# Kernel tuning notes

Hardware: AMD Instinct MI355X
Metric: run time of the kernel (lower is better)

## Reference

```python
import math
import jax, jax.numpy as jnp
import numpy as np

G, NP, L = 256, 24, 3            # graphs, atoms per graph, GPS layers
C, TDIM, NFREQ, NT = 256, 256, 10, 100
EDIM = NFREQ * 2 * 3 + 9         # SinusoidsEmbedding.dim + lattice_input_dim = 69
N = G * NP                       # 6144 nodes
H = 4                            # attention heads


def _silu(x):
    return x * jax.nn.sigmoid(x)


def _bn(x, g, b):
    # BatchNorm1d, training-mode batch statistics (biased var), eps=1e-5
    m = x.mean(0)
    v = ((x - m) ** 2).mean(0)
    return (x - m) * jax.lax.rsqrt(v + 1e-5) * g + b


def _forward(t, frac_coords, lattice, type_emb, node_align_W, node_align_b,
             gine_edge_W, gine_edge_b, gine_W1, gine_b1, gine_W2, gine_b2,
             attn_in_W, attn_in_b, attn_out_W, attn_out_b,
             mlp_W1, mlp_b1, mlp_W2, mlp_b2,
             bn1_g, bn1_b, bn2_g, bn2_b, bn3_g, bn3_b, ln_g, ln_b,
             tro_W1, tro_b1, tro_W2, tro_b2,
             lat_W1, lat_b1, lat_W2, lat_b2, lat_W3,
             fc_W1, fc_b1, fc_W2, fc_b2, fc_W3,
             atom_types, node2graph, edge_src, edge_dst):
    # sinusoidal time embedding [G, TDIM], repeated per node
    half = TDIM // 2
    tf = jnp.exp(jnp.arange(half, dtype=jnp.float32) * (-math.log(10000.0) / (half - 1)))
    te = t[:, None] * tf[None, :]
    te = jnp.concatenate([jnp.sin(te), jnp.cos(te)], -1)
    time_emb = jnp.repeat(te, NP, axis=0)                      # [N, TDIM]
    x = jnp.concatenate([type_emb[atom_types], time_emb], 1) @ node_align_W + node_align_b

    # edge features: sinusoids of periodic frac diff + per-graph lattice
    fd = (frac_coords[edge_dst] - frac_coords[edge_src]) % 1.0  # [E,3]
    sf = 2.0 * math.pi * jnp.arange(NFREQ, dtype=jnp.float32)
    emb = (fd[..., None] * sf).reshape(-1, 3 * NFREQ)
    eattr = jnp.concatenate([jnp.sin(emb), jnp.cos(emb), lattice[node2graph[edge_src]]], 1)

    scale = 1.0 / math.sqrt(C // H)
    for l in range(L):
        # --- GINEConv: gather -> relu(x_j + edge_emb) -> scatter-add -> MLP ---
        eemb = eattr @ gine_edge_W[l] + gine_edge_b[l]          # [E, C]
        msg = jax.nn.relu(x[edge_src] + eemb)
        aggr = jax.ops.segment_sum(msg, edge_dst, num_segments=N)
        z = x + aggr                                            # (1+eps)*x, eps=0
        z = _silu(z @ gine_W1[l] + gine_b1[l]) @ gine_W2[l] + gine_b2[l]
        h1 = _bn(z + x, bn1_g[l], bn1_b[l])
        # --- dense-batched multihead self-attention (all graphs have NP nodes) ---
        xd = x.reshape(G, NP, C)
        qkv = xd @ attn_in_W[l] + attn_in_b[l]
        q, k, v = jnp.split(qkv, 3, axis=-1)
        q = q.reshape(G, NP, H, C // H).transpose(0, 2, 1, 3)
        k = k.reshape(G, NP, H, C // H).transpose(0, 2, 1, 3)
        v = v.reshape(G, NP, H, C // H).transpose(0, 2, 1, 3)
        a = jax.nn.softmax(jnp.einsum('ghqd,ghkd->ghqk', q, k) * scale, axis=-1)
        o = jnp.einsum('ghqk,ghkd->ghqd', a, v).transpose(0, 2, 1, 3).reshape(G, NP, C)
        o = (o @ attn_out_W[l] + attn_out_b[l]).reshape(N, C)
        h2 = _bn(o + x, bn2_g[l], bn2_b[l])
        # --- combine + MLP (GPSConv default: ReLU, dropout=0) ---
        out = h1 + h2
        out = out + jax.nn.relu(out @ mlp_W1[l] + mlp_b1[l]) @ mlp_W2[l] + mlp_b2[l]
        x = _bn(out, bn3_g[l], bn3_b[l])

    # final LayerNorm over feature dim
    m = x.mean(-1, keepdims=True)
    v = ((x - m) ** 2).mean(-1, keepdims=True)
    hn = (x - m) * jax.lax.rsqrt(v + 1e-5) * ln_g + ln_b

    # scatter-mean graph pooling
    cnt = jax.ops.segment_sum(jnp.ones((N, 1), hn.dtype), node2graph, num_segments=G)
    gf = jax.ops.segment_sum(hn, node2graph, num_segments=G) / cnt

    types_pred = _silu(hn @ tro_W1 + tro_b1) @ tro_W2 + tro_b2
    lattice_pred = _silu(_silu(gf @ lat_W1 + lat_b1) @ lat_W2 + lat_b2) @ lat_W3
    frac_pred = _silu(_silu(hn @ fc_W1 + fc_b1) @ fc_W2 + fc_b2) @ fc_W3
    return types_pred, lattice_pred, frac_pred


def setup_inputs() -> dict:
    key = jax.random.key(0)
    ki = iter(jax.random.split(key, 40))

    def nrm(shape, s=0.02):
        return jax.random.normal(next(ki), shape, jnp.float32) * s

    # block-diagonal fully-connected edges, dense_to_sparse row-major order
    g = np.repeat(np.arange(G), NP * NP)
    i = np.tile(np.repeat(np.arange(NP), NP), G)
    j = np.tile(np.tile(np.arange(NP), NP), G)
    inp = {
        "t": jax.random.uniform(next(ki), (G,), jnp.float32),
        "frac_coords": jax.random.uniform(next(ki), (N, 3), jnp.float32),
        "lattice": nrm((G, 9), 1.0),
        "type_emb": nrm((NT, C)),
        "node_align_W": nrm((C + TDIM, C)), "node_align_b": jnp.zeros((C,), jnp.float32),
        "gine_edge_W": nrm((L, EDIM, C)), "gine_edge_b": jnp.zeros((L, C), jnp.float32),
        "gine_W1": nrm((L, C, C)), "gine_b1": jnp.zeros((L, C), jnp.float32),
        "gine_W2": nrm((L, C, C)), "gine_b2": jnp.zeros((L, C), jnp.float32),
        "attn_in_W": nrm((L, C, 3 * C)), "attn_in_b": jnp.zeros((L, 3 * C), jnp.float32),
        "attn_out_W": nrm((L, C, C)), "attn_out_b": jnp.zeros((L, C), jnp.float32),
        "mlp_W1": nrm((L, C, 2 * C)), "mlp_b1": jnp.zeros((L, 2 * C), jnp.float32),
        "mlp_W2": nrm((L, 2 * C, C)), "mlp_b2": jnp.zeros((L, C), jnp.float32),
        "bn1_g": jnp.ones((L, C), jnp.float32), "bn1_b": jnp.zeros((L, C), jnp.float32),
        "bn2_g": jnp.ones((L, C), jnp.float32), "bn2_b": jnp.zeros((L, C), jnp.float32),
        "bn3_g": jnp.ones((L, C), jnp.float32), "bn3_b": jnp.zeros((L, C), jnp.float32),
        "ln_g": jnp.ones((C,), jnp.float32), "ln_b": jnp.zeros((C,), jnp.float32),
        "tro_W1": nrm((C, C // 2)), "tro_b1": jnp.zeros((C // 2,), jnp.float32),
        "tro_W2": nrm((C // 2, NT)), "tro_b2": jnp.zeros((NT,), jnp.float32),
        "lat_W1": nrm((C, C // 2)), "lat_b1": jnp.zeros((C // 2,), jnp.float32),
        "lat_W2": nrm((C // 2, C // 4)), "lat_b2": jnp.zeros((C // 4,), jnp.float32),
        "lat_W3": nrm((C // 4, 9)),
        "fc_W1": nrm((C, C // 2)), "fc_b1": jnp.zeros((C // 2,), jnp.float32),
        "fc_W2": nrm((C // 2, C // 4)), "fc_b2": jnp.zeros((C // 4,), jnp.float32),
        "fc_W3": nrm((C // 4, 3)),
        "atom_types": jax.random.randint(next(ki), (N,), 0, NT, jnp.int32),
        "node2graph": jnp.asarray(np.repeat(np.arange(G), NP), jnp.int32),
        "edge_src": jnp.asarray(g * NP + i, jnp.int32),
        "edge_dst": jnp.asarray(g * NP + j, jnp.int32),
    }
    return inp


def reference(t, frac_coords, lattice, type_emb, node_align_W, node_align_b,
              gine_edge_W, gine_edge_b, gine_W1, gine_b1, gine_W2, gine_b2,
              attn_in_W, attn_in_b, attn_out_W, attn_out_b,
              mlp_W1, mlp_b1, mlp_W2, mlp_b2,
              bn1_g, bn1_b, bn2_g, bn2_b, bn3_g, bn3_b, ln_g, ln_b,
              tro_W1, tro_b1, tro_W2, tro_b2,
              lat_W1, lat_b1, lat_W2, lat_b2, lat_W3,
              fc_W1, fc_b1, fc_W2, fc_b2, fc_W3,
              atom_types, node2graph, edge_src, edge_dst):
    return _forward(t, frac_coords, lattice, type_emb, node_align_W, node_align_b,
                    gine_edge_W, gine_edge_b, gine_W1, gine_b1, gine_W2, gine_b2,
                    attn_in_W, attn_in_b, attn_out_W, attn_out_b,
                    mlp_W1, mlp_b1, mlp_W2, mlp_b2,
                    bn1_g, bn1_b, bn2_g, bn2_b, bn3_g, bn3_b, ln_g, ln_b,
                    tro_W1, tro_b1, tro_W2, tro_b2,
                    lat_W1, lat_b1, lat_W2, lat_b2, lat_W3,
                    fc_W1, fc_b1, fc_W2, fc_b2, fc_W3,
                    atom_types, node2graph, edge_src, edge_dst)
```

## Files before the change

### kernel.cpp

```cpp
#include <hip/hip_runtime.h>
#include <hip/hip_bf16.h>
#include <math.h>

#define GG 256
#define NP 24
#define LL 3
#define CC 256
#define NN (GG*NP)
#define HH 4
#define DH 64

typedef __hip_bfloat16 bf;
typedef __attribute__((ext_vector_type(8))) short bfrag;
typedef __attribute__((ext_vector_type(4))) float ffrag;

__device__ __forceinline__ short pk(float x) {
    union { bf h; short s; } u; u.h = __float2bfloat16(x); return u.s;
}
__device__ __forceinline__ float b2f_s(short x) {
    union { short s; bf h; } u; u.s = x; return __bfloat162float(u.h);
}

typedef __attribute__((address_space(1))) const void gv_t;
typedef __attribute__((address_space(3))) void lv_t;

__global__ void signal_k(float* out, int n, float val) {
    int i = blockIdx.x * 256 + threadIdx.x;
    if (i < n) out[i] = val;
}

struct TArgs {
    const float* src[9];
    long dstOff[9];
    int K[9], N[9], L[9];
    int blk0[10];
};
__global__ void transp_all(TArgs a, bf* __restrict__ wt) {
    int bid = blockIdx.x;
    int s = 0;
    while (s < 8 && bid >= a.blk0[s + 1]) ++s;
    long idx = (long)(bid - a.blk0[s]) * 256 + threadIdx.x;
    int KN = a.K[s] * a.N[s];
    long sz = (long)KN * a.L[s];
    if (idx >= sz) return;
    int l = (int)(idx / KN);
    int rem = (int)(idx % KN);
    int k = rem / a.N[s], n = rem % a.N[s];
    wt[a.dstOff[s] + (long)l * KN + (long)n * a.K[s] + k] =
        __float2bfloat16(a.src[s][idx]);
}

#define ETAB_ELEMS (GG * 24 * 24 * 64)
__global__ void prep_gewtab(const float* __restrict__ geW, short* __restrict__ wh,
                            short* __restrict__ wl, const float* __restrict__ frac,
                            short* __restrict__ eh, short* __restrict__ el) {
    int bid = blockIdx.x;
    if (bid < 192) {
        int idx = bid * 256 + threadIdx.x;
        if (idx >= 49152) return;
        int k = idx & 63;
        int n = (idx >> 6) & 127;
        int half = (idx >> 13) & 1;
        int l = idx >> 14;
        float v = (k < 60) ? geW[(long)l * 69 * 256 + (long)k * 256 + half * 128 + n] : 0.f;
        short hi = pk(v);
        short lo = pk(v - b2f_s(hi));
        wh[idx] = hi;
        wl[idx] = lo;
    } else {
        int idx = (bid - 192) * 256 + threadIdx.x;
        if (idx >= ETAB_ELEMS) return;
        int k = idx & 63;
        int rem = idx >> 6;
        int i = rem % 24;
        int rem2 = rem / 24;
        int j = rem2 % 24;
        int g = rem2 / 24;
        float val = 0.f;
        if (k < 60) {
            int r = (k < 30) ? k : k - 30;
            int d = r / 10, f = r % 10;
            float fd = frac[g * 72 + j * 3 + d] - frac[g * 72 + i * 3 + d];
            fd -= floorf(fd);
            float ang = 6.283185307179586f * (float)f * fd;
            val = (k < 30) ? sinf(ang) : cosf(ang);
        }
        short hi = pk(val);
        eh[idx] = hi;
        el[idx] = pk(val - b2f_s(hi));
    }
}

__global__ void build_A(const float* __restrict__ t, const float* __restrict__ type_emb,
                        const unsigned int* __restrict__ atoms,
                        float* __restrict__ A) {
    __shared__ int ok;
    if (threadIdx.x == 0) ok = 1;
    __syncthreads();
    if (atoms[2 * threadIdx.x + 1] != 0u) ok = 0;
    __syncthreads();
    int i64 = ok;
    int idx = blockIdx.x * 256 + threadIdx.x;
    if (idx >= NN * 512) return;
    int n = idx >> 9;
    int k = idx & 511;
    if (k < 256) {
        int a = i64 ? (int)atoms[2 * n] : (int)atoms[n];
        A[idx] = type_emb[(long)a * CC + k];
    } else {
        int d = k - 256;
        int g = n / NP;
        float tv = t[g];
        int dd = (d < 128) ? d : d - 128;
        float tf = expf(dd * (-9.210340371976184f / 127.0f));
        float ang = tv * tf;
        A[idx] = (d < 128) ? sinf(ang) : cosf(ang);
    }
}

__global__ __launch_bounds__(256) void gemm_mfma(
        const float* __restrict__ A, const bf* __restrict__ Wt,
        const float* __restrict__ bias, const float* __restrict__ bias2,
        const float* __restrict__ res,
        float* __restrict__ C, int M, int K, int N, int act) {
    __shared__ __align__(16) short As[2][32 * 72];
    __shared__ __align__(16) short Bs[2][2][64 * 32];
    int tid = threadIdx.x;
    int lane = tid & 63, w = tid >> 6;
    int wm = w & 1, wn = w >> 1;
    int m0 = blockIdx.x * 32, n0 = blockIdx.y * 64;
    ffrag acc[2] = {};
    int sa_m = tid >> 3, sa_k = (tid & 7) << 3;
    int fr_row = lane & 15, quad = lane >> 4, fr_k = quad << 3;
    int brow = w * 16 + (lane >> 2);
    int bko = (lane & 3) << 3;
    const short* wsrc = (const short*)Wt + (long)(n0 + brow) * K + bko;

    {
        const float* Ap = A + (long)(m0 + sa_m) * K + sa_k;
        float4 a1 = *(const float4*)Ap;
        float4 a2 = *(const float4*)(Ap + 4);
        __builtin_amdgcn_global_load_lds((gv_t*)(wsrc), (lv_t*)(&Bs[0][0][w * 512]), 16, 0, 0);
        __builtin_amdgcn_global_load_lds((gv_t*)(wsrc + 32), (lv_t*)(&Bs[0][1][w * 512]), 16, 0, 0);
        short* ap = &As[0][sa_m * 72 + sa_k];
        ap[0] = pk(a1.x); ap[1] = pk(a1.y); ap[2] = pk(a1.z); ap[3] = pk(a1.w);
        ap[4] = pk(a2.x); ap[5] = pk(a2.y); ap[6] = pk(a2.z); ap[7] = pk(a2.w);
    }
    __syncthreads();

    int nk = K >> 6;
    int cur = 0;
    for (int i = 0; i < nk; ++i) {
        float4 a1n, a2n;
        bool more = (i + 1) < nk;
        if (more) {
            int kn = (i + 1) << 6;
            __builtin_amdgcn_global_load_lds((gv_t*)(wsrc + kn),
                (lv_t*)(&Bs[cur ^ 1][0][w * 512]), 16, 0, 0);
            __builtin_amdgcn_global_load_lds((gv_t*)(wsrc + kn + 32),
                (lv_t*)(&Bs[cur ^ 1][1][w * 512]), 16, 0, 0);
            const float* Ap = A + (long)(m0 + sa_m) * K + kn + sa_k;
            a1n = *(const float4*)Ap;
            a2n = *(const float4*)(Ap + 4);
        }
        bfrag af0  = *(const bfrag*)(&As[cur][(wm * 16 + fr_row) * 72 + fr_k]);
        bfrag af1  = *(const bfrag*)(&As[cur][(wm * 16 + fr_row) * 72 + 32 + fr_k]);
        bfrag bg00 = *(const bfrag*)(&Bs[cur][0][(wn * 32 + fr_row) * 32 + fr_k]);
        bfrag bg01 = *(const bfrag*)(&Bs[cur][0][(wn * 32 + 16 + fr_row) * 32 + fr_k]);
        bfrag bg10 = *(const bfrag*)(&Bs[cur][1][(wn * 32 + fr_row) * 32 + fr_k]);
        bfrag bg11 = *(const bfrag*)(&Bs[cur][1][(wn * 32 + 16 + fr_row) * 32 + fr_k]);
        acc[0] = __builtin_amdgcn_mfma_f32_16x16x32_bf16(af0, bg00, acc[0], 0, 0, 0);
        acc[1] = __builtin_amdgcn_mfma_f32_16x16x32_bf16(af0, bg01, acc[1], 0, 0, 0);
        acc[0] = __builtin_amdgcn_mfma_f32_16x16x32_bf16(af1, bg10, acc[0], 0, 0, 0);
        acc[1] = __builtin_amdgcn_mfma_f32_16x16x32_bf16(af1, bg11, acc[1], 0, 0, 0);
        if (more) {
            short* ap = &As[cur ^ 1][sa_m * 72 + sa_k];
            ap[0] = pk(a1n.x); ap[1] = pk(a1n.y); ap[2] = pk(a1n.z); ap[3] = pk(a1n.w);
            ap[4] = pk(a2n.x); ap[5] = pk(a2n.y); ap[6] = pk(a2n.z); ap[7] = pk(a2n.w);
        }
        __syncthreads();
        cur ^= 1;
    }

    int mbase = (lane >> 4) << 2;
#pragma unroll
    for (int nt = 0; nt < 2; ++nt) {
        int n = n0 + wn * 32 + nt * 16 + (lane & 15);
        float bv = bias ? ((bias2 && n >= 128) ? bias2[n - 128] : bias[n]) : 0.f;
#pragma unroll
        for (int r = 0; r < 4; ++r) {
            int m = m0 + wm * 16 + mbase + r;
            float v = acc[nt][r] + bv;
            if (act == 1) v = fmaxf(v, 0.f);
            else if (act == 2) v = v / (1.f + expf(-v));
            if (res) v += res[(long)m * N + n];
            C[(long)m * N + n] = v;
        }
    }
}

__global__ __launch_bounds__(256) void gemm_k(
        const float* __restrict__ A, int lda, const float* __restrict__ W,
        const float* __restrict__ bias, const float* __restrict__ res,
        float* __restrict__ Cf, int M, int K, int Nc, int act) {
    __shared__ __align__(16) float Asf[32][64];
    __shared__ __align__(16) float Bsf[32][64];
    int tid = threadIdx.x;
    int tx = tid & 15, ty = tid >> 4;
    int m0 = blockIdx.x * 64, n0 = blockIdx.y * 64;
    float acc[4][4] = {{0.f}};
    int am = tid >> 2;
    int ak = (tid & 3) << 3;
    int bk = tid >> 4;
    int bn = (tid & 15) << 2;

    for (int k0 = 0; k0 < K; k0 += 32) {
        const float* Ap = A + (long)(m0 + am) * lda + k0 + ak;
        float4 a1 = *(const float4*)Ap;
        float4 a2 = *(const float4*)(Ap + 4);
        float w1[4], w2[4];
#pragma unroll
        for (int u = 0; u < 4; ++u) {
            int n = n0 + bn + u;
            w1[u] = (n < Nc) ? W[(long)(k0 + bk) * Nc + n] : 0.f;
            w2[u] = (n < Nc) ? W[(long)(k0 + bk + 16) * Nc + n] : 0.f;
        }
        __syncthreads();
        Asf[ak + 0][am] = a1.x; Asf[ak + 1][am] = a1.y;
        Asf[ak + 2][am] = a1.z; Asf[ak + 3][am] = a1.w;
        Asf[ak + 4][am] = a2.x; Asf[ak + 5][am] = a2.y;
        Asf[ak + 6][am] = a2.z; Asf[ak + 7][am] = a2.w;
#pragma unroll
        for (int u = 0; u < 4; ++u) {
            Bsf[bk][bn + u] = w1[u];
            Bsf[bk + 16][bn + u] = w2[u];
        }
        __syncthreads();
#pragma unroll
        for (int k = 0; k < 32; ++k) {
            float4 a = *(const float4*)(&Asf[k][ty << 2]);
            float4 b = *(const float4*)(&Bsf[k][tx << 2]);
            acc[0][0] += a.x * b.x; acc[0][1] += a.x * b.y; acc[0][2] += a.x * b.z; acc[0][3] += a.x * b.w;
            acc[1][0] += a.y * b.x; acc[1][1] += a.y * b.y; acc[1][2] += a.y * b.z; acc[1][3] += a.y * b.w;
            acc[2][0] += a.z * b.x; acc[2][1] += a.z * b.y; acc[2][2] += a.z * b.z; acc[2][3] += a.z * b.w;
            acc[3][0] += a.w * b.x; acc[3][1] += a.w * b.y; acc[3][2] += a.w * b.z; acc[3][3] += a.w * b.w;
        }
    }
#pragma unroll
    for (int i = 0; i < 4; ++i) {
        int m = m0 + (ty << 2) + i;
#pragma unroll
        for (int j = 0; j < 4; ++j) {
            int n = n0 + (tx << 2) + j;
            if (n >= Nc) continue;
            float v = acc[i][j];
            if (bias) v += bias[n];
            if (act == 1) v = fmaxf(v, 0.f);
            else if (act == 2) v = v / (1.f + expf(-v));
            if (res) v += res[(long)m * Nc + n];
            Cf[(long)m * Nc + n] = v;
        }
    }
}

#define MF(a, b, c) c = __builtin_amdgcn_mfma_f32_16x16x32_bf16(a, b, c, 0, 0, 0)

__device__ __forceinline__ void stage_etile(const short* __restrict__ ej_h,
                                            const short* __restrict__ ej_l,
                                            short* lds_base, int w, int lane) {
    {
        int c = w;
        const short* src = (c < 3) ? (ej_h + c * 512) : (ej_l + (c - 3) * 512);
        int doff = (c < 3) ? c * 512 : 2048 + (c - 3) * 512;
        __builtin_amdgcn_global_load_lds((gv_t*)(src + lane * 8),
                                         (lv_t*)(lds_base + doff), 16, 0, 0);
    }
    if (w < 2) {
        int c = w + 4;
        const short* src = ej_l + (c - 3) * 512;
        int doff = 2048 + (c - 3) * 512;
        __builtin_amdgcn_global_load_lds((gv_t*)(src + lane * 8),
                                         (lv_t*)(lds_base + doff), 16, 0, 0);
    }
}

__global__ __launch_bounds__(256, 4) void gine4(
        const float* __restrict__ x,
        const float* __restrict__ lattice, const float* __restrict__ geW,
        const float* __restrict__ geb, const short* __restrict__ gewt_h,
        const short* __restrict__ gewt_l, const short* __restrict__ et_h,
        const short* __restrict__ et_l, float* __restrict__ z, int l) {
    __shared__ __align__(16) float xls[24 * 132];
    __shared__ float basel[128];
    __shared__ __align__(16) short ebuf[8192];

    int tid = threadIdx.x;
    int lane = tid & 63, w = tid >> 6, quad = lane >> 4, l16 = lane & 15;
    int g = blockIdx.x >> 2;
    int half = (blockIdx.x >> 1) & 1;
    int jh = blockIdx.x & 1;

    {
        const float4* xg = (const float4*)x;
        for (int idx = tid; idx < 768; idx += 256) {
            int i = idx >> 5, c4 = idx & 31;
            ((float4*)(xls + i * 132))[c4] =
                xg[((long)(g * NP + i) * CC + half * 128) / 4 + c4];
        }
    }
    if (tid < 128) {
        int cg = half * 128 + tid;
        float bv = geb[(long)l * CC + cg];
#pragma unroll
        for (int q = 0; q < 9; ++q)
            bv += lattice[(long)g * 9 + q] * geW[(long)l * 69 * 256 + (long)(60 + q) * 256 + cg];
        basel[tid] = bv;
    }

    bfrag bh00, bh01, bh10, bh11, bl00, bl01, bl10, bl11;
    {
        long base = (long)(l * 2 + half) * 8192;
        int nrow0 = w * 32 + l16;
        int nrow1 = w * 32 + 16 + l16;
        const short* p0h = gewt_h + base + nrow0 * 64 + quad * 8;
        const short* p1h = gewt_h + base + nrow1 * 64 + quad * 8;
        const short* p0l = gewt_l + base + nrow0 * 64 + quad * 8;
        const short* p1l = gewt_l + base + nrow1 * 64 + quad * 8;
        bh00 = *(const bfrag*)(p0h);      bh01 = *(const bfrag*)(p0h + 32);
        bh10 = *(const bfrag*)(p1h);      bh11 = *(const bfrag*)(p1h + 32);
        bl00 = *(const bfrag*)(p0l);      bl01 = *(const bfrag*)(p0l + 32);
        bl10 = *(const bfrag*)(p1l);      bl11 = *(const bfrag*)(p1l + 32);
    }

    const short* ehg = et_h + (long)g * (24 * 24 * 64);
    const short* elg = et_l + (long)g * (24 * 24 * 64);
    int j0 = jh * 12;

    stage_etile(ehg + (long)j0 * 1536, elg + (long)j0 * 1536, ebuf, w, lane);
    __syncthreads();

    float bse0 = basel[w * 32 + l16];
    float bse1 = basel[w * 32 + 16 + l16];

    int cur = 0;
    for (int jc = 0; jc < 12; ++jc) {
        int j = j0 + jc;
        if (jc < 11) {
            stage_etile(ehg + (long)(j + 1) * 1536, elg + (long)(j + 1) * 1536,
                        ebuf + (cur ^ 1) * 4096, w, lane);
        }

        const short* eb = ebuf + cur * 4096;
        int r0 = l16 * 64 + quad * 8;
        int r1 = (16 + l16) * 64 + quad * 8;
        bfrag ah00 = *(const bfrag*)(eb + r0);
        bfrag ah01 = *(const bfrag*)(eb + r0 + 32);
        bfrag ah10 = *(const bfrag*)(eb + r1);
        bfrag ah11 = *(const bfrag*)(eb + r1 + 32);
        bfrag al00 = *(const bfrag*)(eb + 2048 + r0);
        bfrag al01 = *(const bfrag*)(eb + 2048 + r0 + 32);
        bfrag al10 = *(const bfrag*)(eb + 2048 + r1);
        bfrag al11 = *(const bfrag*)(eb + 2048 + r1 + 32);

        ffrag a00 = {}, a01 = {}, a10 = {}, a11 = {};
        MF(ah00, bh00, a00); MF(ah00, bl00, a00); MF(al00, bh00, a00);
        MF(ah00, bh10, a01); MF(ah00, bl10, a01); MF(al00, bh10, a01);
        MF(ah01, bh01, a00); MF(ah01, bl01, a00); MF(al01, bh01, a00);
        MF(ah01, bh11, a01); MF(ah01, bl11, a01); MF(al01, bh11, a01);
        MF(ah10, bh00, a10); MF(ah10, bl00, a10); MF(al10, bh00, a10);
        MF(ah10, bh10, a11); MF(ah10, bl10, a11); MF(al10, bh10, a11);
        MF(ah11, bh01, a10); MF(ah11, bl01, a10); MF(al11, bh01, a10);
        MF(ah11, bh11, a11); MF(ah11, bl11, a11); MF(al11, bh11, a11);

#pragma unroll
        for (int nt = 0; nt < 2; ++nt) {
            int cl = w * 32 + nt * 16 + l16;
            float bse = nt ? bse1 : bse0;
            ffrag am0 = nt ? a01 : a00;
            ffrag am1 = nt ? a11 : a10;
            float part = 0.f;
            {
                int ibase = quad * 4;
#pragma unroll
                for (int r = 0; r < 4; ++r) {
                    float xv = xls[(ibase + r) * 132 + cl];
                    part += fmaxf(xv + bse + am0[r], 0.f);
                }
            }
            if (quad < 2) {
                int ibase = 16 + quad * 4;
#pragma unroll
                for (int r = 0; r < 4; ++r) {
                    float xv = xls[(ibase + r) * 132 + cl];
                    part += fmaxf(xv + bse + am1[r], 0.f);
                }
            }
            part += __shfl_xor(part, 16);
            part += __shfl_xor(part, 32);
            if (lane < 16)
                z[(long)(g * NP + j) * CC + half * 128 + cl] = xls[j * 132 + cl] + part;
        }
        __syncthreads();
        cur ^= 1;
    }
}

__global__ void bn_stats1(const float* __restrict__ in, float* __restrict__ part) {
    int c = threadIdx.x, b = blockIdx.x;
    float s = 0.f, q = 0.f;
    for (int r = 0; r < 64; ++r) {
        float v = in[(long)(b * 64 + r) * CC + c];
        s += v; q += v * v;
    }
    part[b * 512 + c] = s;
    part[b * 512 + 256 + c] = q;
}
__global__ __launch_bounds__(256) void bn_apply2(
        const float* __restrict__ in, const float* __restrict__ part,
        const float* __restrict__ gma, const float* __restrict__ bta,
        const float* __restrict__ add, float* __restrict__ out) {
    int c = threadIdx.x;
    float s = 0.f, q = 0.f;
    for (int b = 0; b < 96; ++b) { s += part[b * 512 + c]; q += part[b * 512 + 256 + c]; }
    float m = s / (float)NN;
    float var = q / (float)NN - m * m;
    float stats_c = m;
    float stats_rs = rsqrtf(var + 1e-5f);
    float gc = gma[c], bc = bta[c];
    for (int r = blockIdx.x; r < NN; r += 768) {
        long idx = (long)r * CC + c;
        float v = (in[idx] - stats_c) * stats_rs * gc + bc;
        if (add) v += add[idx];
        out[idx] = v;
    }
}

__global__ __launch_bounds__(256, 2) void attn2(const float* __restrict__ qkv,
                                                float* __restrict__ o) {
    __shared__ __align__(16) float Kl[24 * 4 * 68];
    __shared__ __align__(16) float Vl[24 * 4 * 68];
    __shared__ float S[4 * 24 * 25];
    int tid = threadIdx.x, g = blockIdx.x;

    const float4* qkv4 = (const float4*)(qkv + (long)g * NP * 768);
    for (int idx = tid; idx < 24 * 128; idx += 256) {
        int row = idx >> 7;
        int c4 = idx & 127;
        int isV = c4 >> 6;
        int cc = c4 & 63;
        int h = cc >> 4, d4 = cc & 15;
        float4 val = qkv4[row * 192 + 64 + c4];
        float* dst = (isV ? Vl : Kl) + (row * 4 + h) * 68 + d4 * 4;
        *(float4*)dst = val;
    }
    __syncthreads();

    if (tid < 96) {
        int h = tid & 3, i = tid >> 2;
        const float4* qp = (const float4*)(qkv + ((long)(g * NP + i)) * 768 + h * 64);
        float4 q[16];
#pragma unroll
        for (int k = 0; k < 16; ++k) q[k] = qp[k];
        float sc[24];
        float mx = -1e30f;
        for (int j = 0; j < 24; ++j) {
            const float4* kp = (const float4*)(Kl + (j * 4 + h) * 68);
            float da = 0.f, db = 0.f;
#pragma unroll
            for (int k = 0; k < 16; k += 2) {
                float4 kv = kp[k];
                da += q[k].x * kv.x; da += q[k].y * kv.y;
                da += q[k].z * kv.z; da += q[k].w * kv.w;
                float4 kv2 = kp[k + 1];
                db += q[k + 1].x * kv2.x; db += q[k + 1].y * kv2.y;
                db += q[k + 1].z * kv2.z; db += q[k + 1].w * kv2.w;
            }
            float s = (da + db) * 0.125f;
            sc[j] = s;
            mx = fmaxf(mx, s);
        }
        float sum = 0.f;
#pragma unroll
        for (int j = 0; j < 24; ++j) { float p = expf(sc[j] - mx); sc[j] = p; sum += p; }
        float inv = 1.f / sum;
#pragma unroll
        for (int j = 0; j < 24; ++j) S[(h * 24 + i) * 25 + j] = sc[j] * inv;
    }
    __syncthreads();

    int h = tid >> 6, d = tid & 63;
    for (int i = 0; i < 24; ++i) {
        const float* Sp = S + (h * 24 + i) * 25;
        float a0 = 0.f, a1 = 0.f;
#pragma unroll
        for (int j = 0; j < 24; j += 2) {
            a0 += Sp[j] * Vl[(j * 4 + h) * 68 + d];
            a1 += Sp[j + 1] * Vl[((j + 1) * 4 + h) * 68 + d];
        }
        o[(long)(g * NP + i) * CC + h * 64 + d] = a0 + a1;
    }
}

__global__ __launch_bounds__(256) void ln_kernel(const float* __restrict__ x,
        const float* __restrict__ gma, const float* __restrict__ bta,
        float* __restrict__ out) {
    __shared__ float red[256];
    int n = blockIdx.x, c = threadIdx.x;
    float v = x[(long)n * CC + c];
    red[c] = v;
    __syncthreads();
    for (int s = 128; s > 0; s >>= 1) { if (c < s) red[c] += red[c + s]; __syncthreads(); }
    float m = red[0] * (1.f / 256.f);
    __syncthreads();
    float dv = v - m;
    red[c] = dv * dv;
    __syncthreads();
    for (int s = 128; s > 0; s >>= 1) { if (c < s) red[c] += red[c + s]; __syncthreads(); }
    float var = red[0] * (1.f / 256.f);
    out[(long)n * CC + c] = dv * rsqrtf(var + 1e-5f) * gma[c] + bta[c];
}

__global__ __launch_bounds__(256) void lat_head(
        const float* __restrict__ hn, const float* __restrict__ W1,
        const float* __restrict__ b1, const float* __restrict__ W2,
        const float* __restrict__ b2, const float* __restrict__ W3,
        float* __restrict__ out) {
    __shared__ float gfl[256];
    __shared__ float h1[128];
    __shared__ float h2[64];
    int g = blockIdx.x, t = threadIdx.x;
    {
        float s = 0.f;
        for (int j = 0; j < NP; ++j) s += hn[(long)(g * NP + j) * CC + t];
        gfl[t] = s * (1.f / 24.f);
    }
    __syncthreads();
    if (t < 128) {
        float acc = 0.f;
        for (int k = 0; k < 256; ++k) acc += gfl[k] * W1[k * 128 + t];
        float v = acc;
        v += b1[t];
        v = v / (1.f + expf(-v));
        h1[t] = v;
    }
    __syncthreads();
    if (t < 64) {
        float acc = 0.f;
        for (int k = 0; k < 128; ++k) acc += h1[k] * W2[k * 64 + t];
        float v = acc;
        v += b2[t];
        v = v / (1.f + expf(-v));
        h2[t] = v;
    }
    __syncthreads();
    if (t < 9) {
        float acc = 0.f;
        for (int k = 0; k < 64; ++k) acc += h2[k] * W3[k * 9 + t];
        out[(long)g * 9 + t] = acc;
    }
}

static void gemm(hipStream_t st, const float* A, int lda, const float* W,
                 const float* bias, const float* res, float* Cf,
                 int M, int K, int Nc, int act) {
    dim3 grid(M / 64, (Nc + 63) / 64);
    gemm_k<<<grid, 256, 0, st>>>(A, lda, W, bias, res, Cf, M, K, Nc, act);
}

static void gemmM(hipStream_t st, const float* A, const bf* Wt, const float* bias,
                  const float* bias2, const float* res, float* Cf,
                  int M, int K, int N, int act) {
    dim3 grid(M / 32, N / 64);
    gemm_mfma<<<grid, 256, 0, st>>>(A, Wt, bias, bias2, res, Cf, M, K, N, act);
}

static void run_bn(hipStream_t st, const float* in, float* part,
                   const float* g_, const float* b_, const float* add, float* out) {
    bn_stats1<<<96, 256, 0, st>>>(in, part);
    bn_apply2<<<768, 256, 0, st>>>(in, part, g_, b_, add, out);
}

extern "C" void kernel_launch(void* const* d_in, const int* in_sizes, int n_in,
                              void* d_out, int out_size, void* d_ws, size_t ws_size,
                              hipStream_t stream) {
    float* out = (float*)d_out;
    int sigN = out_size < 256 ? out_size : 256;

    static const int EXP_SIZES[46] = {
        256, 18432, 2304, 25600, 131072, 256, 52992, 768, 196608, 768,
        196608, 768, 589824, 2304, 196608, 768, 393216, 1536, 393216, 768,
        768, 768, 768, 768, 768, 768, 256, 256, 32768, 128,
        12800, 100, 32768, 128, 8192, 64, 576, 32768, 128, 8192,
        64, 192, 6144, 6144, 147456, 147456 };
    if (n_in != 46) { signal_k<<<1, 256, 0, stream>>>(out, sigN, 3000.f + 8.f * n_in); return; }
    for (int i = 0; i < 46; ++i)
        if (in_sizes[i] != EXP_SIZES[i]) { signal_k<<<1, 256, 0, stream>>>(out, sigN, 512.f + 8.f * i); return; }
    if (out_size != NN * 100 + GG * 9 + NN * 3) { signal_k<<<1, 256, 0, stream>>>(out, sigN, 7777.f); return; }

    char* base = (char*)d_ws;
    float* f32a = (float*)(base + 256);
    float* x  = f32a;
    float* s1 = x  + (size_t)NN * 256;
    float* s2 = s1 + (size_t)NN * 256;
    float* big = s2 + (size_t)NN * 256;
    float* s3 = big + (size_t)NN * 512;
    float* part = big + (size_t)NN * 768;
    float* stats = part + 96 * 512;
    float* gf  = stats + 512;
    float* l1b = gf + GG * 256;
    float* l2b = l1b + GG * 128;
    bf* wt = (bf*)(l2b + GG * 64);
    const long O_NA = 0, O_G1 = 131072, O_G2 = 327680, O_AI = 524288,
               O_AO = 1114112, O_M1 = 1310720, O_M2 = 1703936,
               O_TRO = 2097152, O_FC = 2129920, WT_TOT = 2162688;
    short* gewt_h = (short*)(wt + WT_TOT);
    short* gewt_l = gewt_h + 49152;
    short* et_h = gewt_l + 49152;
    short* et_l = et_h + (ETAB_ELEMS + 1024);
    size_t REQ = 256 + ((size_t)NN * 1536 + 96 * 512 + 512 + GG * 448) * 4
               + WT_TOT * 2 + 49152 * 2 * 2
               + ((size_t)ETAB_ELEMS + 1024) * 2 * 2;
    if (ws_size < REQ) { signal_k<<<1, 256, 0, stream>>>(out, sigN, 9999.f); return; }

    const float* t       = (const float*)d_in[0];
    const float* frac    = (const float*)d_in[1];
    const float* lattice = (const float*)d_in[2];
    const float* type_emb = (const float*)d_in[3];

    {
        TArgs ta;
        const int srcIdx[9] = {4, 8, 10, 12, 14, 16, 18, 28, 37};
        const long dof[9]  = {O_NA, O_G1, O_G2, O_AI, O_AO, O_M1, O_M2, O_TRO, O_FC};
        const int Ks[9] = {512, 256, 256, 256, 256, 256, 512, 256, 256};
        const int Ns[9] = {256, 256, 256, 768, 256, 512, 256, 128, 128};
        const int Ls[9] = {1, 3, 3, 3, 3, 3, 3, 1, 1};
        int blk = 0;
        for (int s = 0; s < 9; ++s) {
            ta.src[s] = (const float*)d_in[srcIdx[s]];
            ta.dstOff[s] = dof[s];
            ta.K[s] = Ks[s]; ta.N[s] = Ns[s]; ta.L[s] = Ls[s];
            ta.blk0[s] = blk;
            blk += (Ks[s] * Ns[s] * Ls[s] + 255) / 256;
        }
        ta.blk0[9] = blk;
        transp_all<<<blk, 256, 0, stream>>>(ta, wt);
    }
    prep_gewtab<<<192 + (ETAB_ELEMS + 255) / 256, 256, 0, stream>>>(
        (const float*)d_in[6], gewt_h, gewt_l, frac, et_h, et_l);

    build_A<<<(NN * 512 + 255) / 256, 256, 0, stream>>>(t, type_emb,
        (const unsigned int*)d_in[42], big);
    gemmM(stream, big, wt + O_NA, (const float*)d_in[5], nullptr, nullptr, x, NN, 512, 256, 0);

    for (int l = 0; l < LL; ++l) {
        gine4<<<GG * 4, 256, 0, stream>>>(x, lattice,
            (const float*)d_in[6], (const float*)d_in[7], gewt_h, gewt_l,
            et_h, et_l, s1, l);
        gemmM(stream, s1, wt + O_G1 + (long)l * 65536, (const float*)d_in[9]  + l * 256, nullptr, nullptr, s2, NN, 256, 256, 2);
        gemmM(stream, s2, wt + O_G2 + (long)l * 65536, (const float*)d_in[11] + l * 256, nullptr, x, s3, NN, 256, 256, 0);
        run_bn(stream, s3, part, (const float*)d_in[20] + l * 256, (const float*)d_in[21] + l * 256, nullptr, s2);
        gemmM(stream, x, wt + O_AI + (long)l * 196608, (const float*)d_in[13] + l * 768, nullptr, nullptr, big, NN, 256, 768, 0);
        attn2<<<GG, 256, 0, stream>>>(big, s1);
        gemmM(stream, s1, wt + O_AO + (long)l * 65536, (const float*)d_in[15] + l * 256, nullptr, x, s3, NN, 256, 256, 0);
        run_bn(stream, s3, part, (const float*)d_in[22] + l * 256, (const float*)d_in[23] + l * 256, s2, s1);
        gemmM(stream, s1, wt + O_M1 + (long)l * 131072, (const float*)d_in[17] + l * 512, nullptr, nullptr, big, NN, 256, 512, 1);
        gemmM(stream, big, wt + O_M2 + (long)l * 131072, (const float*)d_in[19] + l * 256, nullptr, s1, s3, NN, 512, 256, 0);
        run_bn(stream, s3, part, (const float*)d_in[24] + l * 256, (const float*)d_in[25] + l * 256, nullptr, x);
    }

    ln_kernel<<<NN, 256, 0, stream>>>(x, (const float*)d_in[26], (const float*)d_in[27], s1);

    gemmM(stream, s1, wt + O_TRO, (const float*)d_in[29], (const float*)d_in[38],
          nullptr, s2, NN, 256, 256, 2);
    gemm(stream, s2, 256, (const float*)d_in[30], (const float*)d_in[31], nullptr, out, NN, 128, 100, 0);
    lat_head<<<GG, 256, 0, stream>>>(s1, (const float*)d_in[32], (const float*)d_in[33],
        (const float*)d_in[34], (const float*)d_in[35], (const float*)d_in[36],
        out + (size_t)NN * 100);
    gemm(stream, s2 + 128, 256, (const float*)d_in[39], (const float*)d_in[40], nullptr, s3, NN, 128, 64, 2);
    gemm(stream, s3, 64, (const float*)d_in[41], nullptr, nullptr, out + (size_t)NN * 100 + GG * 9, NN, 64, 3, 0);
}
```

Baseline: 708.5 us.

## Merge prep kernels into one launch and fuse output heads into a tail kernel

Three setup kernels (weight transposes, edge-table prep, input-row build) are folded into one launch that dispatches on block index. The four output-stage launches (type head GEMM, frac head two-layer MLP, lattice head) become one tail kernel. In the frac head the 64-wide hidden layer stays in shared memory instead of going through global memory. This cuts launch count and one global round trip, but the tail kernel uses more shared memory per block, and blocks within the fused launches are unbalanced.

Measured after the change: 676.2 us. -4.6%, faster.

```diff
diff --git a/kernel.cpp b/kernel.cpp
--- a/kernel.cpp
+++ b/kernel.cpp
@@ -29,92 +29,99 @@
     if (i < n) out[i] = val;
 }
 
+#define ETAB_ELEMS (GG * 24 * 24 * 64)
+#define GEWTAB_BLKS (192 + (ETAB_ELEMS + 255) / 256)
+#define BUILDA_BLKS ((NN * 512 + 255) / 256)
+
 struct TArgs {
     const float* src[9];
     long dstOff[9];
     int K[9], N[9], L[9];
     int blk0[10];
 };
-__global__ void transp_all(TArgs a, bf* __restrict__ wt) {
+
+__global__ void prep_all(TArgs a, bf* __restrict__ wt,
+                         const float* __restrict__ geW, short* __restrict__ wh,
+                         short* __restrict__ wl, const float* __restrict__ frac,
+                         short* __restrict__ eh, short* __restrict__ el,
+                         const float* __restrict__ t,
+                         const float* __restrict__ type_emb,
+                         const unsigned int* __restrict__ atoms,
+                         float* __restrict__ A) {
+    __shared__ int ok;
     int bid = blockIdx.x;
-    int s = 0;
-    while (s < 8 && bid >= a.blk0[s + 1]) ++s;
-    long idx = (long)(bid - a.blk0[s]) * 256 + threadIdx.x;
-    int KN = a.K[s] * a.N[s];
-    long sz = (long)KN * a.L[s];
-    if (idx >= sz) return;
-    int l = (int)(idx / KN);
-    int rem = (int)(idx % KN);
-    int k = rem / a.N[s], n = rem % a.N[s];
-    wt[a.dstOff[s] + (long)l * KN + (long)n * a.K[s] + k] =
-        __float2bfloat16(a.src[s][idx]);
-}
-
-#define ETAB_ELEMS (GG * 24 * 24 * 64)
-__global__ void prep_gewtab(const float* __restrict__ geW, short* __restrict__ wh,
-                            short* __restrict__ wl, const float* __restrict__ frac,
-                            short* __restrict__ eh, short* __restrict__ el) {
-    int bid = blockIdx.x;
-    if (bid < 192) {
-        int idx = bid * 256 + threadIdx.x;
-        if (idx >= 49152) return;
-        int k = idx & 63;
-        int n = (idx >> 6) & 127;
-        int half = (idx >> 13) & 1;
-        int l = idx >> 14;
-        float v = (k < 60) ? geW[(long)l * 69 * 256 + (long)k * 256 + half * 128 + n] : 0.f;
-        short hi = pk(v);
-        short lo = pk(v - b2f_s(hi));
-        wh[idx] = hi;
-        wl[idx] = lo;
+    int nT = a.blk0[9];
+    if (bid < nT) {
+        int s = 0;
+        while (s < 8 && bid >= a.blk0[s + 1]) ++s;
+        long idx = (long)(bid - a.blk0[s]) * 256 + threadIdx.x;
+        int KN = a.K[s] * a.N[s];
+        long sz = (long)KN * a.L[s];
+        if (idx >= sz) return;
+        int l = (int)(idx / KN);
+        int rem = (int)(idx % KN);
+        int k = rem / a.N[s], n = rem % a.N[s];
+        wt[a.dstOff[s] + (long)l * KN + (long)n * a.K[s] + k] =
+            __float2bfloat16(a.src[s][idx]);
+    } else if (bid < nT + GEWTAB_BLKS) {
+        int b2 = bid - nT;
+        if (b2 < 192) {
+            int idx = b2 * 256 + threadIdx.x;
+            if (idx >= 49152) return;
+            int k = idx & 63;
+            int n = (idx >> 6) & 127;
+            int half = (idx >> 13) & 1;
+            int l = idx >> 14;
+            float v = (k < 60) ? geW[(long)l * 69 * 256 + (long)k * 256 + half * 128 + n] : 0.f;
+            short hi = pk(v);
+            short lo = pk(v - b2f_s(hi));
+            wh[idx] = hi;
+            wl[idx] = lo;
+        } else {
+            int idx = (b2 - 192) * 256 + threadIdx.x;
+            if (idx >= ETAB_ELEMS) return;
+            int k = idx & 63;
+            int rem = idx >> 6;
+            int i = rem % 24;
+            int rem2 = rem / 24;
+            int j = rem2 % 24;
+            int g = rem2 / 24;
+            float val = 0.f;
+            if (k < 60) {
+                int r = (k < 30) ? k : k - 30;
+                int d = r / 10, f = r % 10;
+                float fd = frac[g * 72 + j * 3 + d] - frac[g * 72 + i * 3 + d];
+                fd -= floorf(fd);
+                float ang = 6.283185307179586f * (float)f * fd;
+                val = (k < 30) ? sinf(ang) : cosf(ang);
+            }
+            short hi = pk(val);
+            eh[idx] = hi;
+            el[idx] = pk(val - b2f_s(hi));
+        }
     } else {
-        int idx = (bid - 192) * 256 + threadIdx.x;
-        if (idx >= ETAB_ELEMS) return;
-        int k = idx & 63;
-        int rem = idx >> 6;
-        int i = rem % 24;
-        int rem2 = rem / 24;
-        int j = rem2 % 24;
-        int g = rem2 / 24;
-        float val = 0.f;
-        if (k < 60) {
-            int r = (k < 30) ? k : k - 30;
-            int d = r / 10, f = r % 10;
-            float fd = frac[g * 72 + j * 3 + d] - frac[g * 72 + i * 3 + d];
-            fd -= floorf(fd);
-            float ang = 6.283185307179586f * (float)f * fd;
-            val = (k < 30) ? sinf(ang) : cosf(ang);
-        }
-        short hi = pk(val);
-        eh[idx] = hi;
-        el[idx] = pk(val - b2f_s(hi));
-    }
-}
-
-__global__ void build_A(const float* __restrict__ t, const float* __restrict__ type_emb,
-                        const unsigned int* __restrict__ atoms,
-                        float* __restrict__ A) {
-    __shared__ int ok;
-    if (threadIdx.x == 0) ok = 1;
-    __syncthreads();
-    if (atoms[2 * threadIdx.x + 1] != 0u) ok = 0;
-    __syncthreads();
-    int i64 = ok;
-    int idx = blockIdx.x * 256 + threadIdx.x;
-    if (idx >= NN * 512) return;
-    int n = idx >> 9;
-    int k = idx & 511;
-    if (k < 256) {
-        int a = i64 ? (int)atoms[2 * n] : (int)atoms[n];
-        A[idx] = type_emb[(long)a * CC + k];
-    } else {
-        int d = k - 256;
-        int g = n / NP;
-        float tv = t[g];
-        int dd = (d < 128) ? d : d - 128;
-        float tf = expf(dd * (-9.210340371976184f / 127.0f));
-        float ang = tv * tf;
-        A[idx] = (d < 128) ? sinf(ang) : cosf(ang);
+        int b3 = bid - nT - GEWTAB_BLKS;
+        if (threadIdx.x == 0) ok = 1;
+        __syncthreads();
+        if (atoms[2 * threadIdx.x + 1] != 0u) ok = 0;
+        __syncthreads();
+        int i64 = ok;
+        int idx = b3 * 256 + threadIdx.x;
+        if (idx >= NN * 512) return;
+        int n = idx >> 9;
+        int k = idx & 511;
+        if (k < 256) {
+            int aidx = i64 ? (int)atoms[2 * n] : (int)atoms[n];
+            A[idx] = type_emb[(long)aidx * CC + k];
+        } else {
+            int d = k - 256;
+            int g = n / NP;
+            float tv = t[g];
+            int dd = (d < 128) ? d : d - 128;
+            float tf = expf(dd * (-9.210340371976184f / 127.0f));
+            float ang = tv * tf;
+            A[idx] = (d < 128) ? sinf(ang) : cosf(ang);
+        }
     }
 }
 
@@ -199,15 +206,13 @@
     }
 }
 
-__global__ __launch_bounds__(256) void gemm_k(
-        const float* __restrict__ A, int lda, const float* __restrict__ W,
-        const float* __restrict__ bias, const float* __restrict__ res,
-        float* __restrict__ Cf, int M, int K, int Nc, int act) {
-    __shared__ __align__(16) float Asf[32][64];
-    __shared__ __align__(16) float Bsf[32][64];
-    int tid = threadIdx.x;
+__device__ __forceinline__ void gemm_k_body(
+        const float* __restrict__ A, int lda, int mA0,
+        const float* __restrict__ W, const float* __restrict__ bias,
+        float* __restrict__ Cf, int ldc, int mOut0,
+        int n0, int K, int Nc, int act,
+        float (*Asf)[64], float (*Bsf)[64], int tid) {
     int tx = tid & 15, ty = tid >> 4;
-    int m0 = blockIdx.x * 64, n0 = blockIdx.y * 64;
     float acc[4][4] = {{0.f}};
     int am = tid >> 2;
     int ak = (tid & 3) << 3;
@@ -215,7 +220,7 @@
     int bn = (tid & 15) << 2;
 
     for (int k0 = 0; k0 < K; k0 += 32) {
-        const float* Ap = A + (long)(m0 + am) * lda + k0 + ak;
+        const float* Ap = A + (long)(mA0 + am) * lda + k0 + ak;
         float4 a1 = *(const float4*)Ap;
         float4 a2 = *(const float4*)(Ap + 4);
         float w1[4], w2[4];
@@ -248,7 +253,7 @@
     }
 #pragma unroll
     for (int i = 0; i < 4; ++i) {
-        int m = m0 + (ty << 2) + i;
+        int m = mOut0 + (ty << 2) + i;
 #pragma unroll
         for (int j = 0; j < 4; ++j) {
             int n = n0 + (tx << 2) + j;
@@ -257,8 +262,70 @@
             if (bias) v += bias[n];
             if (act == 1) v = fmaxf(v, 0.f);
             else if (act == 2) v = v / (1.f + expf(-v));
-            if (res) v += res[(long)m * Nc + n];
-            Cf[(long)m * Nc + n] = v;
+            Cf[(long)m * ldc + n] = v;
+        }
+    }
+}
+
+__global__ __launch_bounds__(256) void tail_k(
+        const float* __restrict__ s2, const float* __restrict__ s1,
+        const float* __restrict__ W30, const float* __restrict__ b31,
+        const float* __restrict__ W39, const float* __restrict__ b40,
+        const float* __restrict__ W41,
+        const float* __restrict__ lw1, const float* __restrict__ lb1,
+        const float* __restrict__ lw2, const float* __restrict__ lb2,
+        const float* __restrict__ lw3,
+        float* __restrict__ out_types, float* __restrict__ out_lat,
+        float* __restrict__ out_frac) {
+    __shared__ __align__(16) float Asf[32][64];
+    __shared__ __align__(16) float Bsf[32][64];
+    __shared__ __align__(16) float Imm[64][64];
+    __shared__ float gfl[256];
+    __shared__ float h1s[128];
+    __shared__ float h2s[64];
+    int tid = threadIdx.x;
+    int b = blockIdx.x;
+    if (b < 192) {
+        int bx = b >> 1, by = b & 1;
+        gemm_k_body(s2, 256, bx * 64, W30, b31, out_types, 100, bx * 64,
+                    by * 64, 128, 100, 0, Asf, Bsf, tid);
+    } else if (b < 288) {
+        int m0 = (b - 192) * 64;
+        gemm_k_body(s2 + 128, 256, m0, W39, b40, &Imm[0][0], 64, 0,
+                    0, 128, 64, 2, Asf, Bsf, tid);
+        __syncthreads();
+        gemm_k_body(&Imm[0][0], 64, 0, W41, nullptr, out_frac, 3, m0,
+                    0, 64, 3, 0, Asf, Bsf, tid);
+    } else {
+        int g = b - 288, t = tid;
+        {
+            float s = 0.f;
+            for (int j = 0; j < NP; ++j) s += s1[(long)(g * NP + j) * CC + t];
+            gfl[t] = s * (1.f / 24.f);
+        }
+        __syncthreads();
+        if (t < 128) {
+            float acc = 0.f;
+            for (int k = 0; k < 256; ++k) acc += gfl[k] * lw1[k * 128 + t];
+            float v = acc;
+            v += lb1[t];
+            v = v / (1.f + expf(-v));
+            h1s[t] = v;
+        }
+        __syncthreads();
+        if (t < 64) {
+            float acc = 0.f;
+            for (int k = 0; k < 128; ++k) acc += h1s[k] * lw2[k * 64 + t];
+            float v = acc;
+            v += lb2[t];
+            v = v / (1.f + expf(-v));
+            h2s[t] = v;
+        }
+        __syncthreads();
+        if (t < 9) {
+            float acc = 0.f;
+            for (int k = 0; k < 64; ++k) acc += h2s[k] * lw3[k * 9 + t];
+            out_lat[(long)g * 9 + t] = acc;
         }
     }
 }
@@ -518,53 +585,6 @@
     for (int s = 128; s > 0; s >>= 1) { if (c < s) red[c] += red[c + s]; __syncthreads(); }
     float var = red[0] * (1.f / 256.f);
     out[(long)n * CC + c] = dv * rsqrtf(var + 1e-5f) * gma[c] + bta[c];
-}
-
-__global__ __launch_bounds__(256) void lat_head(
-        const float* __restrict__ hn, const float* __restrict__ W1,
-        const float* __restrict__ b1, const float* __restrict__ W2,
-        const float* __restrict__ b2, const float* __restrict__ W3,
-        float* __restrict__ out) {
-    __shared__ float gfl[256];
-    __shared__ float h1[128];
-    __shared__ float h2[64];
-    int g = blockIdx.x, t = threadIdx.x;
-    {
-        float s = 0.f;
-        for (int j = 0; j < NP; ++j) s += hn[(long)(g * NP + j) * CC + t];
-        gfl[t] = s * (1.f / 24.f);
-    }
-    __syncthreads();
-    if (t < 128) {
-        float acc = 0.f;
-        for (int k = 0; k < 256; ++k) acc += gfl[k] * W1[k * 128 + t];
-        float v = acc;
-        v += b1[t];
-        v = v / (1.f + expf(-v));
-        h1[t] = v;
-    }
-    __syncthreads();
-    if (t < 64) {
-        float acc = 0.f;
-        for (int k = 0; k < 128; ++k) acc += h1[k] * W2[k * 64 + t];
-        float v = acc;
-        v += b2[t];
-        v = v / (1.f + expf(-v));
-        h2[t] = v;
-    }
-    __syncthreads();
-    if (t < 9) {
-        float acc = 0.f;
-        for (int k = 0; k < 64; ++k) acc += h2[k] * W3[k * 9 + t];
-        out[(long)g * 9 + t] = acc;
-    }
-}
-
-static void gemm(hipStream_t st, const float* A, int lda, const float* W,
-                 const float* bias, const float* res, float* Cf,
-                 int M, int K, int Nc, int act) {
-    dim3 grid(M / 64, (Nc + 63) / 64);
-    gemm_k<<<grid, 256, 0, st>>>(A, lda, W, bias, res, Cf, M, K, Nc, act);
 }
 
 static void gemmM(hipStream_t st, const float* A, const bf* Wt, const float* bias,
@@ -627,6 +647,7 @@
     const float* lattice = (const float*)d_in[2];
     const float* type_emb = (const float*)d_in[3];
 
+    int nTblk;
     {
         TArgs ta;
         const int srcIdx[9] = {4, 8, 10, 12, 14, 16, 18, 28, 37};
@@ -643,13 +664,12 @@
             blk += (Ks[s] * Ns[s] * Ls[s] + 255) / 256;
         }
         ta.blk0[9] = blk;
-        transp_all<<<blk, 256, 0, stream>>>(ta, wt);
-    }
-    prep_gewtab<<<192 + (ETAB_ELEMS + 255) / 256, 256, 0, stream>>>(
-        (const float*)d_in[6], gewt_h, gewt_l, frac, et_h, et_l);
-
-    build_A<<<(NN * 512 + 255) / 256, 256, 0, stream>>>(t, type_emb,
-        (const unsigned int*)d_in[42], big);
+        nTblk = blk;
+        prep_all<<<nTblk + GEWTAB_BLKS + BUILDA_BLKS, 256, 0, stream>>>(
+            ta, wt, (const float*)d_in[6], gewt_h, gewt_l, frac, et_h, et_l,
+            t, type_emb, (const unsigned int*)d_in[42], big);
+    }
+
     gemmM(stream, big, wt + O_NA, (const float*)d_in[5], nullptr, nullptr, x, NN, 512, 256, 0);
 
     for (int l = 0; l < LL; ++l) {
@@ -672,10 +692,10 @@
 
     gemmM(stream, s1, wt + O_TRO, (const float*)d_in[29], (const float*)d_in[38],
           nullptr, s2, NN, 256, 256, 2);
-    gemm(stream, s2, 256, (const float*)d_in[30], (const float*)d_in[31], nullptr, out, NN, 128, 100, 0);
-    lat_head<<<GG, 256, 0, stream>>>(s1, (const float*)d_in[32], (const float*)d_in[33],
+    tail_k<<<544, 256, 0, stream>>>(s2, s1,
+        (const float*)d_in[30], (const float*)d_in[31],
+        (const float*)d_in[39], (const float*)d_in[40], (const float*)d_in[41],
+        (const float*)d_in[32], (const float*)d_in[33],
         (const float*)d_in[34], (const float*)d_in[35], (const float*)d_in[36],
-        out + (size_t)NN * 100);
-    gemm(stream, s2 + 128, 256, (const float*)d_in[39], (const float*)d_in[40], nullptr, s3, NN, 128, 64, 2);
-    gemm(stream, s3, 64, (const float*)d_in[41], nullptr, nullptr, out + (size_t)NN * 100 + GG * 9, NN, 64, 3, 0);
-}
+        out, out + (size_t)NN * 100, out + (size_t)NN * 100 + GG * 9);
+}
```
